# Performance work log

Hardware: AMD Instinct MI355X
Metric: run time of the kernel (lower is better)

## Reference

```python
import jax, jax.numpy as jnp
import numpy as np

NBX = 24  # nb_x_patches
NBY = 24  # nb_y_patches
B, H, D = 8, 12, 64
L = NBX * NBY + 1  # 577 (grid tokens + 1 CLS token from the pad)
EPS = 1e-08


def _toeplitz_mask(topological_params):
    # topological_params: [H, 4*NBX*NBY]
    gi = jnp.arange(NBX)
    gj = jnp.arange(NBY)
    # relative 2D displacement index, flattened over (i, j, i', j')
    dist_index = ((gi[:, None, None, None] - gi[None, None, :, None] + NBX) * 2 * NBY
                  + gj[None, :, None, None] - gj[None, None, None, :] + NBY)
    dist_index = dist_index.reshape(-1)
    m = jnp.take(topological_params, dist_index, axis=1)
    m = m.reshape(topological_params.shape[0], NBX * NBY, NBX * NBY)  # [H, L-1, L-1]
    # pad CLS row and column with 1.0
    m = jnp.pad(m, [[0, 0], [1, 0], [1, 0]], constant_values=1.0)  # [H, L, L]
    return m[None]  # [1, H, L, L]


def setup_inputs() -> dict:
    key = jax.random.key(0)
    k1, k2, k3, k4 = jax.random.split(key, 4)
    return {
        'query': jax.random.normal(k1, (B, L, H, D), dtype=jnp.float32),
        'key': jax.random.normal(k2, (B, L, H, D), dtype=jnp.float32),
        'value': jax.random.normal(k3, (B, L, H, D), dtype=jnp.float32),
        'topological_params': jax.random.normal(k4, (H, 4 * NBX * NBY), dtype=jnp.float32),
    }


def reference(query, key, value, topological_params):
    depth = query.shape[-1]
    q = query / jnp.sqrt(jnp.asarray(depth, query.dtype))
    # relu feature map (kernel_type == 'relu')
    q = jax.nn.relu(q) + EPS
    k = jax.nn.relu(key) + EPS
    attn = jnp.einsum('bqhd,bkhd->bhqk', q, k)  # [B, H, L, L]
    top_mask = _toeplitz_mask(topological_params)  # [1, H, L, L]
    attn = attn * jnp.abs(top_mask) + EPS
    attn = attn / jnp.sum(attn, axis=-1, keepdims=True)  # kernelized normalization (no softmax)
    return jnp.einsum('bhqk,bkhd->bqhd', attn, value)
```

## Files before the change

kernel.cpp:

```cpp
#include <hip/hip_runtime.h>


#define Lq 577
#define NH 12
#define NB 8
#define DD 64
#define PAR 2304
#define EPSf 1e-8f

#define VT_OFF 7090176ull
#define MM_OFF 14954496ull

#define PK_BLOCKS  1731
#define PVT_BLOCKS 960
#define PM_BLOCKS  2316

typedef __attribute__((ext_vector_type(4))) float f32x4;
typedef __attribute__((ext_vector_type(8))) short s16x8;

__device__ __forceinline__ float bflo(unsigned int u) {
    return __builtin_bit_cast(float, u << 16);
}
__device__ __forceinline__ float bfhi(unsigned int u) {
    return __builtin_bit_cast(float, u & 0xffff0000u);
}
__device__ __forceinline__ unsigned int f2bf(float f) {
    unsigned int x = __builtin_bit_cast(unsigned int, f);
    return (x + 0x7fffu + ((x >> 16) & 1u)) >> 16;
}
__device__ __forceinline__ int imin(int a, int b) { return a < b ? a : b; }

__device__ __forceinline__ void gload_lds16(const unsigned short* g, unsigned short* l) {
    __builtin_amdgcn_global_load_lds(
        (const __attribute__((address_space(1))) unsigned int*)g,
        (__attribute__((address_space(3))) unsigned int*)l, 16, 0, 0);
}

__device__ __forceinline__ bool probe_f32(const void* Qg) {
    float x = fabsf(((const float*)Qg)[threadIdx.x]);
    unsigned long long hit = __ballot(x > 2.44140625e-4f && x < 64.0f);
    unsigned long long act = __ballot(1);
    return 2 * __popcll(hit) >= __popcll(act);
}

template <bool F32>
__device__ __forceinline__ void load8f(const void* G, size_t eidx, float* o) {
    if constexpr (F32) {
        const float* p = (const float*)G + eidx;
        float4 a = *(const float4*)p;
        float4 b = *(const float4*)(p + 4);
        o[0] = a.x; o[1] = a.y; o[2] = a.z; o[3] = a.w;
        o[4] = b.x; o[5] = b.y; o[6] = b.z; o[7] = b.w;
    } else {
        const unsigned short* p = (const unsigned short*)G + eidx;
        uint4 a = *(const uint4*)p;
        unsigned int u[4] = {a.x, a.y, a.z, a.w};
#pragma unroll
        for (int j = 0; j < 4; ++j) {
            o[2 * j]     = bflo(u[j]);
            o[2 * j + 1] = bfhi(u[j]);
        }
    }
}

template <bool F32>
__device__ void prep_all_body(const void* __restrict__ Kg,
                              const void* __restrict__ Vg,
                              const void* __restrict__ Tg,
                              unsigned short* __restrict__ Kp,
                              unsigned short* __restrict__ Vt,
                              unsigned short* __restrict__ Mm,
                              unsigned short* s) {
    const int bid = blockIdx.x;
    const int t   = threadIdx.x;

    if (bid < PK_BLOCKS) {
        size_t i8 = ((size_t)bid * 256 + t) * 8;
        float f[8];
        load8f<F32>(Kg, i8, f);
        unsigned int o[4];
#pragma unroll
        for (int j = 0; j < 4; ++j) {
            unsigned int lo = f2bf(fmaxf(f[2 * j], 0.0f) + EPSf);
            unsigned int hi = f2bf(fmaxf(f[2 * j + 1], 0.0f) + EPSf);
            o[j] = lo | (hi << 16);
        }
        *(uint4*)(Kp + i8) = make_uint4(o[0], o[1], o[2], o[3]);

    } else if (bid < PK_BLOCKS + PVT_BLOCKS) {
        int r  = bid - PK_BLOCKS;
        int kt = r % 10; r /= 10;
        int h  = r % NH;
        int b  = r / NH;
        {
            int kl  = t >> 2;
            int dch = (t & 3) * 16;
            int k   = kt * 64 + kl;
            unsigned int pk[8] = {};
            if (k <= 576) {
                float f[16];
                size_t base = ((size_t)((b * Lq + k) * NH + h)) * DD + dch;
                load8f<F32>(Vg, base, f);
                load8f<F32>(Vg, base + 8, f + 8);
#pragma unroll
                for (int j = 0; j < 8; ++j)
                    pk[j] = f2bf(f[2 * j]) | (f2bf(f[2 * j + 1]) << 16);
            }
#pragma unroll
            for (int j = 0; j < 8; ++j)
                *(unsigned int*)&s[kl * 72 + dch + 2 * j] = pk[j];
        }
        __syncthreads();
        {
            int d   = t >> 2;
            int kch = (t & 3) * 16;
            unsigned int o[8];
#pragma unroll
            for (int j = 0; j < 8; ++j) {
                unsigned short v0 = s[(kch + 2 * j) * 72 + d];
                unsigned short v1 = s[(kch + 2 * j + 1) * 72 + d];
                o[j] = (unsigned int)v0 | ((unsigned int)v1 << 16);
            }
            size_t base = ((size_t)((b * NH + h) * 64 + d)) * 640 + kt * 64 + kch;
            *(uint4*)(Vt + base)     = make_uint4(o[0], o[1], o[2], o[3]);
            *(uint4*)(Vt + base + 8) = make_uint4(o[4], o[5], o[6], o[7]);
        }

    } else {
        int r  = bid - (PK_BLOCKS + PVT_BLOCKS);
        int h  = r / 193;
        int qb = (r % 193) * 3;
        if (t < 240) {
            int q = qb + t / 80;
            if (q < Lq) {
                int k0 = (t % 80) * 8;
                int cq = 0;
                if (q > 0) {
                    int qq = q - 1;
                    int qi = (qq * 2731) >> 16;
                    cq = qq + 24 * qi + 1176;
                }
                unsigned int o[4];
#pragma unroll
                for (int j = 0; j < 4; ++j) {
                    unsigned int hv[2];
#pragma unroll
                    for (int e = 0; e < 2; ++e) {
                        int k = k0 + 2 * j + e;
                        float m;
                        if (k > 576) m = 0.0f;
                        else if (k == 0 || q == 0) m = 1.0f;
                        else {
                            int kk = k - 1;
                            int ki = (kk * 2731) >> 16;
                            int idx = cq - (kk + 24 * ki);
                            float pv = F32 ? ((const float*)Tg)[h * PAR + idx]
                                           : bflo((unsigned int)((const unsigned short*)Tg)[h * PAR + idx]);
                            m = fabsf(pv);
                            m = (m == m) ? m : 0.0f;
                        }
                        hv[e] = f2bf(m);
                    }
                    o[j] = hv[0] | (hv[1] << 16);
                }
                *(uint4*)(Mm + (size_t)(h * Lq + q) * 640 + k0) = make_uint4(o[0], o[1], o[2], o[3]);
            }
        }
    }
}
__global__ __launch_bounds__(256)
void prep_all(const void* __restrict__ Qg, const void* __restrict__ Kg,
              const void* __restrict__ Vg, const void* __restrict__ Tg,
              unsigned short* __restrict__ Kp, unsigned short* __restrict__ Vt,
              unsigned short* __restrict__ Mm) {
    __shared__ __align__(16) unsigned short s[64 * 72];
    if (probe_f32(Qg)) prep_all_body<true>(Kg, Vg, Tg, Kp, Vt, Mm, s);
    else               prep_all_body<false>(Kg, Vg, Tg, Kp, Vt, Mm, s);
}

template <bool F32>
__device__ void attn_body(const void* __restrict__ Qg,
                          const unsigned short* __restrict__ Kp,
                          const unsigned short* __restrict__ Vt,
                          const unsigned short* __restrict__ Mm,
                          void* __restrict__ Og,
                          unsigned short* s_k, unsigned short* s_vt,
                          unsigned short* s_p_all) {
    const int tid  = threadIdx.x;
    const int w    = tid >> 6;
    const int lane = tid & 63;
    const int g    = lane >> 4;
    const int lm   = lane & 15;

    const int bid  = blockIdx.x;
    const int slot = (bid & 7) * 120 + (bid >> 3);
    const int h    = slot / 80;
    const int rem  = slot - h * 80;
    const int b    = rem / 10;
    const int qt   = rem - b * 10;

    unsigned short* s_pw = s_p_all + w * 16 * 64;
    const int q0w = qt * 64 + w * 16;

    const int q  = q0w + lm;
    const int qc = imin(q, Lq - 1);
    s16x8 a_q[2];
    {
        size_t rbase = ((size_t)((b * Lq + qc) * NH + h)) * DD;
#pragma unroll
        for (int ds = 0; ds < 2; ++ds) {
            float f[8];
            load8f<F32>(Qg, rbase + ds * 32 + g * 8, f);
            s16x8 a;
#pragma unroll
            for (int j = 0; j < 8; ++j) {
                float v = fmaf(fmaxf(f[j], 0.0f), 0.125f, EPSf);
                a[j] = (short)f2bf(v);
            }
            a_q[ds] = a;
        }
    }

    const int r8 = lane >> 3;
    const int c8 = lane & 7;
    const int xr = (c8 ^ r8) * 8;

    const unsigned short* KpBH = Kp + (size_t)b * (Lq * NH * DD) + h * DD;
    const unsigned short* VtL0 = Vt + ((size_t)(b * NH + h) * 64 + (w * 16 + r8)) * 640 + xr;
    const unsigned short* VtL1 = VtL0 + 8 * 640;
    const unsigned short* MmQ  = Mm + (size_t)h * (Lq * 640) + (size_t)qc * 640 + g * 4;

    f32x4 o_acc[4] = {};
    float rs = 0.0f;
    const int x7 = lm & 7;

    auto stageKV = [&](int kb, int buf) {
        unsigned short* skb = s_k  + buf * 4096 + (w * 16) * 64;
        unsigned short* svb = s_vt + buf * 4096 + (w * 16) * 64;
        int krr = kb + w * 16 + r8;
        int kr0 = imin(krr, Lq - 1);
        int kr1 = imin(krr + 8, Lq - 1);
        gload_lds16(KpBH + (size_t)kr0 * (NH * DD) + xr, skb);
        gload_lds16(KpBH + (size_t)kr1 * (NH * DD) + xr, skb + 8 * 64);
        gload_lds16(VtL0 + kb, svb);
        gload_lds16(VtL1 + kb, svb + 8 * 64);
    };

    stageKV(0, 0);
    uint2 mu_n[4];
#pragma unroll
    for (int cf = 0; cf < 4; ++cf)
        mu_n[cf] = *(const uint2*)(MmQ + cf * 16);
    __syncthreads();

    for (int t = 0; t < 10; ++t) {
        const int kb  = t * 64;
        const int buf = t & 1;

        uint2 mu[4];
#pragma unroll
        for (int cf = 0; cf < 4; ++cf) mu[cf] = mu_n[cf];

        if (t < 9) {
            stageKV(kb + 64, buf ^ 1);
#pragma unroll
            for (int cf = 0; cf < 4; ++cf)
                mu_n[cf] = *(const uint2*)(MmQ + kb + 64 + cf * 16);
        }

        const unsigned short* skB = s_k  + buf * 4096;
        const unsigned short* svB = s_vt + buf * 4096;

        f32x4 sf[4];
#pragma unroll
        for (int cf = 0; cf < 4; ++cf) {
            const unsigned short* skr = skB + (cf * 16 + lm) * 64;
            int co = (g ^ x7) * 8;
            s16x8 kf0 = *(const s16x8*)(skr + co);
            s16x8 kf1 = *(const s16x8*)(skr + (co ^ 32));
            f32x4 acc = {};
            acc = __builtin_amdgcn_mfma_f32_16x16x32_bf16(kf0, a_q[0], acc, 0, 0, 0);
            acc = __builtin_amdgcn_mfma_f32_16x16x32_bf16(kf1, a_q[1], acc, 0, 0, 0);
            sf[cf] = acc;
        }

#pragma unroll
        for (int cf = 0; cf < 4; ++cf) {
            float m0 = bflo(mu[cf].x), m1 = bfhi(mu[cf].x);
            float m2 = bflo(mu[cf].y), m3 = bfhi(mu[cf].y);
            float p0 = fmaf(fmaxf(sf[cf][0], 0.0f), m0, EPSf);
            float p1 = fmaf(fmaxf(sf[cf][1], 0.0f), m1, EPSf);
            float p2 = fmaf(fmaxf(sf[cf][2], 0.0f), m2, EPSf);
            float p3 = fmaf(fmaxf(sf[cf][3], 0.0f), m3, EPSf);
            rs += (p0 + p1) + (p2 + p3);
            unsigned int d0 = f2bf(p0) | (f2bf(p1) << 16);
            unsigned int d1 = f2bf(p2) | (f2bf(p3) << 16);
            int pc = (((cf * 2 + (g >> 1)) ^ x7) << 3) + ((g & 1) << 2);
            *(uint2*)&s_pw[lm * 64 + pc] = make_uint2(d0, d1);
        }

#pragma unroll
        for (int ks = 0; ks < 2; ++ks) {
            s16x8 pa = *(const s16x8*)&s_pw[lm * 64 + (((ks * 4 + g) ^ x7) << 3)];
#pragma unroll
            for (int df = 0; df < 4; ++df) {
                const unsigned short* svr = svB + (df * 16 + lm) * 64;
                s16x8 vb = *(const s16x8*)(svr + (((ks * 4 + g) ^ x7) << 3));
                o_acc[df] = __builtin_amdgcn_mfma_f32_16x16x32_bf16(pa, vb, o_acc[df], 0, 0, 0);
            }
        }

        if (t < 9) __syncthreads();
    }

    float tot = rs;
    tot += __shfl_xor(tot, 16, 64);
    tot += __shfl_xor(tot, 32, 64);
    float inv = (tot > 0.0f) ? 1.0f / tot : 0.0f;

#pragma unroll
    for (int r = 0; r < 4; ++r) {
        int   qrow  = q0w + g * 4 + r;
        float inv_r = __shfl(inv, g * 4 + r, 64);
        if (qrow < Lq) {
            size_t base = ((size_t)((b * Lq + qrow) * NH + h)) * DD;
#pragma unroll
            for (int df = 0; df < 4; ++df) {
                float val = o_acc[df][r] * inv_r;
                if constexpr (F32)
                    ((float*)Og)[base + df * 16 + lm] = val;
                else
                    ((unsigned short*)Og)[base + df * 16 + lm] = (unsigned short)f2bf(val);
            }
        }
    }
}

__global__ __launch_bounds__(256, 4)
void fused_topo_attn(const void* __restrict__ Qg,
                     const unsigned short* __restrict__ Kp,
                     const unsigned short* __restrict__ Vt,
                     const unsigned short* __restrict__ Mm,
                     void* __restrict__ Og) {
    __shared__ __align__(16) unsigned short s_k[2 * 64 * 64];
    __shared__ __align__(16) unsigned short s_vt[2 * 64 * 64];
    __shared__ __align__(16) unsigned short s_p[4 * 16 * 64];

    if (probe_f32(Qg)) attn_body<true>(Qg, Kp, Vt, Mm, Og, s_k, s_vt, s_p);
    else               attn_body<false>(Qg, Kp, Vt, Mm, Og, s_k, s_vt, s_p);
}

extern "C" void kernel_launch(void* const* d_in, const int* in_sizes, int n_in,
                              void* d_out, int out_size, void* d_ws, size_t ws_size,
                              hipStream_t stream) {
    (void)in_sizes; (void)n_in; (void)out_size; (void)ws_size;
    unsigned short* Kp = (unsigned short*)d_ws;
    unsigned short* Vt = (unsigned short*)((char*)d_ws + VT_OFF);
    unsigned short* Mm = (unsigned short*)((char*)d_ws + MM_OFF);

    prep_all<<<PK_BLOCKS + PVT_BLOCKS + PM_BLOCKS, 256, 0, stream>>>(
        d_in[0], d_in[1], d_in[2], d_in[3], Kp, Vt, Mm);
    fused_topo_attn<<<960, 256, 0, stream>>>(d_in[0], Kp, Vt, Mm, d_out);
}
```

Measured before the change: 126.9 us.

## Keep P in registers via 16x16x16 MFMA, re-swizzle Vt, and trim last key tile

The softmax-free probability tile is now passed straight from the QK accumulator registers into 16x16x16 bf16 MFMAs, so the per-wave LDS round trip for P is gone. The Vt layout written by the prep kernel is re-swizzled at 4-element granularity to match the new B-operand read pattern. The last key tile, which has only one valid key (576), is peeled so that only one 16-column fragment is computed instead of four. In exchange the PV product uses twice as many smaller MFMA instructions, and correctness depends on the new swizzle matching in both kernels.

```diff
diff --git a/kernel.cpp b/kernel.cpp
--- a/kernel.cpp
+++ b/kernel.cpp
@@ -17,6 +17,7 @@
 
 typedef __attribute__((ext_vector_type(4))) float f32x4;
 typedef __attribute__((ext_vector_type(8))) short s16x8;
+typedef __attribute__((ext_vector_type(4))) short s16x4;
 
 __device__ __forceinline__ float bflo(unsigned int u) {
     return __builtin_bit_cast(float, u << 16);
@@ -29,6 +30,16 @@
     return (x + 0x7fffu + ((x >> 16) & 1u)) >> 16;
 }
 __device__ __forceinline__ int imin(int a, int b) { return a < b ? a : b; }
+
+__device__ __forceinline__ f32x4 mfma16(s16x4 a, s16x4 b, f32x4 c) {
+#if __has_builtin(__builtin_amdgcn_mfma_f32_16x16x16bf16_1k)
+    return __builtin_amdgcn_mfma_f32_16x16x16bf16_1k(a, b, c, 0, 0, 0);
+#else
+    s16x8 az = {a[0], a[1], a[2], a[3], 0, 0, 0, 0};
+    s16x8 bz = {b[0], b[1], b[2], b[3], 0, 0, 0, 0};
+    return __builtin_amdgcn_mfma_f32_16x16x32_bf16(az, bz, c, 0, 0, 0);
+#endif
+}
 
 __device__ __forceinline__ void gload_lds16(const unsigned short* g, unsigned short* l) {
     __builtin_amdgcn_global_load_lds(
@@ -121,9 +132,14 @@
                 unsigned short v1 = s[(kch + 2 * j + 1) * 72 + d];
                 o[j] = (unsigned int)v0 | ((unsigned int)v1 << 16);
             }
-            size_t base = ((size_t)((b * NH + h) * 64 + d)) * 640 + kt * 64 + kch;
-            *(uint4*)(Vt + base)     = make_uint4(o[0], o[1], o[2], o[3]);
-            *(uint4*)(Vt + base + 8) = make_uint4(o[4], o[5], o[6], o[7]);
+            size_t rowbase = ((size_t)((b * NH + h) * 64 + d)) * 640 + kt * 64;
+            int swz = d & 15;
+#pragma unroll
+            for (int i = 0; i < 4; ++i) {
+                int c8 = (kch >> 2) + i;
+                *(uint2*)(Vt + rowbase + (size_t)((c8 ^ swz) << 2)) =
+                    make_uint2(o[2 * i], o[2 * i + 1]);
+            }
         }
 
     } else {
@@ -184,8 +200,7 @@
                           const unsigned short* __restrict__ Vt,
                           const unsigned short* __restrict__ Mm,
                           void* __restrict__ Og,
-                          unsigned short* s_k, unsigned short* s_vt,
-                          unsigned short* s_p_all) {
+                          unsigned short* s_k, unsigned short* s_vt) {
     const int tid  = threadIdx.x;
     const int w    = tid >> 6;
     const int lane = tid & 63;
@@ -199,7 +214,6 @@
     const int b    = rem / 10;
     const int qt   = rem - b * 10;
 
-    unsigned short* s_pw = s_p_all + w * 16 * 64;
     const int q0w = qt * 64 + w * 16;
 
     const int q  = q0w + lm;
@@ -226,7 +240,7 @@
     const int xr = (c8 ^ r8) * 8;
 
     const unsigned short* KpBH = Kp + (size_t)b * (Lq * NH * DD) + h * DD;
-    const unsigned short* VtL0 = Vt + ((size_t)(b * NH + h) * 64 + (w * 16 + r8)) * 640 + xr;
+    const unsigned short* VtL0 = Vt + ((size_t)(b * NH + h) * 64 + (w * 16 + r8)) * 640 + c8 * 8;
     const unsigned short* VtL1 = VtL0 + 8 * 640;
     const unsigned short* MmQ  = Mm + (size_t)h * (Lq * 640) + (size_t)qc * 640 + g * 4;
 
@@ -253,7 +267,7 @@
         mu_n[cf] = *(const uint2*)(MmQ + cf * 16);
     __syncthreads();
 
-    for (int t = 0; t < 10; ++t) {
+    for (int t = 0; t < 9; ++t) {
         const int kb  = t * 64;
         const int buf = t & 1;
 
@@ -261,12 +275,10 @@
 #pragma unroll
         for (int cf = 0; cf < 4; ++cf) mu[cf] = mu_n[cf];
 
-        if (t < 9) {
-            stageKV(kb + 64, buf ^ 1);
-#pragma unroll
-            for (int cf = 0; cf < 4; ++cf)
-                mu_n[cf] = *(const uint2*)(MmQ + kb + 64 + cf * 16);
-        }
+        stageKV(kb + 64, buf ^ 1);
+#pragma unroll
+        for (int cf = 0; cf < 4; ++cf)
+            mu_n[cf] = *(const uint2*)(MmQ + kb + 64 + cf * 16);
 
         const unsigned short* skB = s_k  + buf * 4096;
         const unsigned short* svB = s_vt + buf * 4096;
@@ -284,6 +296,7 @@
             sf[cf] = acc;
         }
 
+        s16x4 pa[4];
 #pragma unroll
         for (int cf = 0; cf < 4; ++cf) {
             float m0 = bflo(mu[cf].x), m1 = bfhi(mu[cf].x);
@@ -295,22 +308,50 @@
             rs += (p0 + p1) + (p2 + p3);
             unsigned int d0 = f2bf(p0) | (f2bf(p1) << 16);
             unsigned int d1 = f2bf(p2) | (f2bf(p3) << 16);
-            int pc = (((cf * 2 + (g >> 1)) ^ x7) << 3) + ((g & 1) << 2);
-            *(uint2*)&s_pw[lm * 64 + pc] = make_uint2(d0, d1);
-        }
-
-#pragma unroll
-        for (int ks = 0; ks < 2; ++ks) {
-            s16x8 pa = *(const s16x8*)&s_pw[lm * 64 + (((ks * 4 + g) ^ x7) << 3)];
+            pa[cf] = __builtin_bit_cast(s16x4, make_uint2(d0, d1));
+        }
+
+#pragma unroll
+        for (int cf = 0; cf < 4; ++cf) {
 #pragma unroll
             for (int df = 0; df < 4; ++df) {
-                const unsigned short* svr = svB + (df * 16 + lm) * 64;
-                s16x8 vb = *(const s16x8*)(svr + (((ks * 4 + g) ^ x7) << 3));
-                o_acc[df] = __builtin_amdgcn_mfma_f32_16x16x32_bf16(pa, vb, o_acc[df], 0, 0, 0);
-            }
-        }
-
-        if (t < 9) __syncthreads();
+                const unsigned short* svr =
+                    svB + (df * 16 + lm) * 64 + (((4 * cf + g) ^ lm) << 2);
+                s16x4 vb = __builtin_bit_cast(s16x4, *(const uint2*)svr);
+                o_acc[df] = mfma16(pa[cf], vb, o_acc[df]);
+            }
+        }
+
+        __syncthreads();
+    }
+
+    {
+        const unsigned short* skB = s_k  + 4096;
+        const unsigned short* svB = s_vt + 4096;
+        const unsigned short* skr = skB + lm * 64;
+        int co = (g ^ x7) * 8;
+        s16x8 kf0 = *(const s16x8*)(skr + co);
+        s16x8 kf1 = *(const s16x8*)(skr + (co ^ 32));
+        f32x4 acc = {};
+        acc = __builtin_amdgcn_mfma_f32_16x16x32_bf16(kf0, a_q[0], acc, 0, 0, 0);
+        acc = __builtin_amdgcn_mfma_f32_16x16x32_bf16(kf1, a_q[1], acc, 0, 0, 0);
+        float m0 = bflo(mu_n[0].x), m1 = bfhi(mu_n[0].x);
+        float m2 = bflo(mu_n[0].y), m3 = bfhi(mu_n[0].y);
+        float p0 = fmaf(fmaxf(acc[0], 0.0f), m0, EPSf);
+        float p1 = fmaf(fmaxf(acc[1], 0.0f), m1, EPSf);
+        float p2 = fmaf(fmaxf(acc[2], 0.0f), m2, EPSf);
+        float p3 = fmaf(fmaxf(acc[3], 0.0f), m3, EPSf);
+        rs += (p0 + p1) + (p2 + p3);
+        unsigned int d0 = f2bf(p0) | (f2bf(p1) << 16);
+        unsigned int d1 = f2bf(p2) | (f2bf(p3) << 16);
+        s16x4 pa0 = __builtin_bit_cast(s16x4, make_uint2(d0, d1));
+#pragma unroll
+        for (int df = 0; df < 4; ++df) {
+            const unsigned short* svr =
+                svB + (df * 16 + lm) * 64 + (((g ^ lm)) << 2);
+            s16x4 vb = __builtin_bit_cast(s16x4, *(const uint2*)svr);
+            o_acc[df] = mfma16(pa0, vb, o_acc[df]);
+        }
     }
 
     float tot = rs;
@@ -344,10 +385,9 @@
                      void* __restrict__ Og) {
     __shared__ __align__(16) unsigned short s_k[2 * 64 * 64];
     __shared__ __align__(16) unsigned short s_vt[2 * 64 * 64];
-    __shared__ __align__(16) unsigned short s_p[4 * 16 * 64];
-
-    if (probe_f32(Qg)) attn_body<true>(Qg, Kp, Vt, Mm, Og, s_k, s_vt, s_p);
-    else               attn_body<false>(Qg, Kp, Vt, Mm, Og, s_k, s_vt, s_p);
+
+    if (probe_f32(Qg)) attn_body<true>(Qg, Kp, Vt, Mm, Og, s_k, s_vt);
+    else               attn_body<false>(Qg, Kp, Vt, Mm, Og, s_k, s_vt);
 }
 
 extern "C" void kernel_launch(void* const* d_in, const int* in_sizes, int n_in,
```

After: 123.9 us. 2.3% less time.
